# Kernel tuning notes

Measured on AMD Instinct MI355X. Metric: run time of the kernel, lower is better.

## Reference

```python
import jax, jax.numpy as jnp
import numpy as np

B, H, T, DH = 2, 16, 2048, 64
SCALE = DH ** -0.5


def setup_inputs() -> dict:
    key = jax.random.key(0)
    kq, kk, kv = jax.random.split(key, 3)
    q = jax.random.normal(kq, (B, H, T, DH), dtype=jnp.float32)
    k = jax.random.normal(kk, (B, H, T, DH), dtype=jnp.float32)
    v = jax.random.normal(kv, (B, H, T, DH), dtype=jnp.float32)
    attention_mask = jnp.ones((B, T), dtype=bool)  # (B, Tk) padding mask, True=keep
    causal_mask = jnp.tril(jnp.ones((T, T), dtype=bool))[None, None]  # (1,1,Tq,Tk)
    return {"q": q, "k": k, "v": v, "attention_mask": attention_mask,
            "causal_mask": causal_mask}


def _attend(q, k, v, attention_mask, causal_mask):
    # scores in fp32 as in the torch module
    scores = jnp.einsum("bhqd,bhkd->bhqk", q.astype(jnp.float32),
                        k.astype(jnp.float32)) * SCALE
    neg_inf = jnp.float32(-jnp.inf)
    # (B,Tk) bool padding mask -> (B,1,1,Tk), broadcasts over Tq
    pad = attention_mask[:, None, None, :]
    scores = jnp.where(pad, scores, neg_inf)
    scores = jnp.where(causal_mask, scores, neg_inf)
    attn = jax.nn.softmax(scores, axis=-1).astype(q.dtype)
    ctx = jnp.einsum("bhqk,bhkd->bhqd", attn, v)  # (B,H,Tq,Dh)
    Bq, Hq, Tq, Dh = ctx.shape
    return ctx.transpose(0, 2, 1, 3).reshape(Bq, Tq, Hq * Dh)


def reference(q, k, v, attention_mask, causal_mask):
    return _attend(q, k, v, attention_mask, causal_mask)
```

## Files before the change

kernel.cpp:

```cpp
#include <hip/hip_runtime.h>


constexpr int Bc = 2, Hc = 16, Tc = 2048, Dc = 64;
constexpr float QSCALE = 0.125f * 1.44269504088896340736f;

typedef __attribute__((__ext_vector_type__(8))) __bf16 bf16x8;
typedef __attribute__((__ext_vector_type__(4))) __bf16 bf16x4;
typedef __attribute__((__ext_vector_type__(4))) float f32x4;

__global__ __launch_bounds__(256, 4) void attn_fwd_kernel(
    const float* __restrict__ Q,
    const float* __restrict__ K,
    const float* __restrict__ V,
    float* __restrict__ O)
{
  const int tid  = threadIdx.x;
  const int wave = tid >> 6;
  const int lane = tid & 63;
  const int l16  = lane & 15;
  const int g    = lane >> 4;

  const int bid  = blockIdx.x;
  const int head = bid & 31;
  const int pr   = bid >> 5;
  const int b = head >> 4, h = head & 15;

  const size_t hoff = (size_t)head * Tc * Dc;
  const float* Qb = Q + hoff;
  const float* Kb = K + hoff;
  const float* Vb = V + hoff;

  __shared__ __bf16 Kl[64 * 64];
  __shared__ __bf16 Vt[64 * 64];

  const int krow = tid >> 2;
  const int seg  = tid & 3;
  const int kswz = (krow & 7) << 4;
  const int vkb  = tid >> 4;
  const int vdb  = tid & 15;
  const int vwx  = (vdb >> 2) << 3;

  float4 kreg[4], vreg[4];

  for (int ph = 0; ph < 2; ++ph) {
    const int qtile = ph ? (31 - pr) : pr;
    const int q0 = qtile * 64 + wave * 16;

    bf16x8 qf[2];
    {
      const float4* qp = (const float4*)(Qb + (size_t)(q0 + l16) * Dc + g * 8);
      #pragma unroll
      for (int c = 0; c < 2; ++c) {
        float4 x0 = qp[c * 8], x1 = qp[c * 8 + 1];
        const float* f0 = (const float*)&x0;
        const float* f1 = (const float*)&x1;
        #pragma unroll
        for (int j = 0; j < 4; ++j) {
          qf[c][j]     = (__bf16)(f0[j] * QSCALE);
          qf[c][4 + j] = (__bf16)(f1[j] * QSCALE);
        }
      }
    }

    f32x4 o_acc[4] = {};
    float m_run = -1e30f, l_run = 0.f;

    const int n_iter = qtile + 1;

    {
      const float4* kp4 = (const float4*)(Kb + (size_t)krow * Dc + seg * 16);
      #pragma unroll
      for (int c = 0; c < 4; ++c) kreg[c] = kp4[c];
      const float* vb0 = Vb + (size_t)(vkb * 4) * Dc + vdb * 4;
      #pragma unroll
      for (int r = 0; r < 4; ++r) vreg[r] = *(const float4*)(vb0 + r * Dc);
    }

    for (int it = 0; it < n_iter; ++it) {
      __syncthreads();

      #pragma unroll
      for (int hh = 0; hh < 2; ++hh) {
        const float* x0 = (const float*)&kreg[2 * hh];
        const float* x1 = (const float*)&kreg[2 * hh + 1];
        bf16x8 t;
        #pragma unroll
        for (int j = 0; j < 4; ++j) { t[j] = (__bf16)x0[j]; t[4 + j] = (__bf16)x1[j]; }
        *(bf16x8*)((char*)Kl + krow * 128 + ((seg * 32 + hh * 16) ^ kswz)) = t;
      }
      #pragma unroll
      for (int i = 0; i < 4; ++i) {
        bf16x4 t;
        #pragma unroll
        for (int r = 0; r < 4; ++r) t[r] = (__bf16)((const float*)&vreg[r])[i];
        const int d = vdb * 4 + i;
        *(bf16x4*)((char*)Vt + vkb * 512 + ((d * 8) ^ (vkb << 3) ^ vwx)) = t;
      }
      __syncthreads();

      if (it + 1 < n_iter) {
        const int kv1 = (it + 1) * 64;
        const float4* kp4 = (const float4*)(Kb + (size_t)(kv1 + krow) * Dc + seg * 16);
        #pragma unroll
        for (int c = 0; c < 4; ++c) kreg[c] = kp4[c];
        const float* vb0 = Vb + (size_t)(kv1 + vkb * 4) * Dc + vdb * 4;
        #pragma unroll
        for (int r = 0; r < 4; ++r) vreg[r] = *(const float4*)(vb0 + r * Dc);
      }

      const bool partial = (it == qtile);
      const int  ns = partial ? (wave + 1) : 4;

      f32x4 sacc[4];
      __builtin_amdgcn_s_setprio(1);
      #pragma unroll
      for (int s = 0; s < 4; ++s) {
        if (s < ns) {
          f32x4 z = {0.f, 0.f, 0.f, 0.f};
          const int row = s * 16 + l16;
          const char* kb = (const char*)Kl + row * 128;
          const int swz = (row & 7) << 4;
          bf16x8 k0 = *(const bf16x8*)(kb + ((g * 16) ^ swz));
          bf16x8 k1 = *(const bf16x8*)(kb + ((64 + g * 16) ^ swz));
          z = __builtin_amdgcn_mfma_f32_16x16x32_bf16(k0, qf[0], z, 0, 0, 0);
          z = __builtin_amdgcn_mfma_f32_16x16x32_bf16(k1, qf[1], z, 0, 0, 0);
          sacc[s] = z;
        } else {
          sacc[s] = f32x4{-INFINITY, -INFINITY, -INFINITY, -INFINITY};
        }
      }
      __builtin_amdgcn_s_setprio(0);
      if (partial) {
        #pragma unroll
        for (int s = 0; s < 4; ++s)
          #pragma unroll
          for (int r = 0; r < 4; ++r)
            if (s * 16 + g * 4 + r > wave * 16 + l16) sacc[s][r] = -INFINITY;
      }

      float mx = -INFINITY;
      #pragma unroll
      for (int s = 0; s < 4; ++s)
        #pragma unroll
        for (int r = 0; r < 4; ++r) mx = fmaxf(mx, sacc[s][r]);
      mx = fmaxf(mx, __shfl_xor(mx, 16, 64));
      mx = fmaxf(mx, __shfl_xor(mx, 32, 64));

      if (!__all(mx <= m_run + 8.0f)) {
        const float mn = fmaxf(m_run, mx);
        const float f  = __builtin_amdgcn_exp2f(m_run - mn);
        m_run = mn;
        l_run *= f;
        #pragma unroll
        for (int r = 0; r < 4; ++r) {
          const float fo = __shfl(f, g * 4 + r, 64);
          #pragma unroll
          for (int dt = 0; dt < 4; ++dt) o_acc[dt][r] *= fo;
        }
      }

      float sum = 0.f;
      bf16x8 pa[2];
      #pragma unroll
      for (int c = 0; c < 2; ++c)
        #pragma unroll
        for (int j = 0; j < 8; ++j) {
          const float pv = __builtin_amdgcn_exp2f(sacc[2 * c + (j >> 2)][j & 3] - m_run);
          sum += pv;
          pa[c][j] = (__bf16)pv;
        }
      sum += __shfl_xor(sum, 16, 64);
      sum += __shfl_xor(sum, 32, 64);
      l_run += sum;

      __builtin_amdgcn_s_setprio(1);
      #pragma unroll
      for (int dt = 0; dt < 4; ++dt) {
        const int d = dt * 16 + l16;
        const int dx = (dt & 3) << 3;
        #pragma unroll
        for (int c = 0; c < 2; ++c) {
          const int kc0 = 8 * c + g;
          const int kc1 = 8 * c + 4 + g;
          union { bf16x8 v8; bf16x4 v4[2]; } u;
          u.v4[0] = *(const bf16x4*)((char*)Vt + kc0 * 512 + ((d * 8) ^ (kc0 << 3) ^ dx));
          u.v4[1] = *(const bf16x4*)((char*)Vt + kc1 * 512 + ((d * 8) ^ (kc1 << 3) ^ dx));
          o_acc[dt] = __builtin_amdgcn_mfma_f32_16x16x32_bf16(pa[c], u.v8, o_acc[dt], 0, 0, 0);
        }
      }
      __builtin_amdgcn_s_setprio(0);
    }

    #pragma unroll
    for (int r = 0; r < 4; ++r) {
      const float il = __shfl(l_run, g * 4 + r, 64);
      const float inv = 1.f / il;
      float* orow = O + ((size_t)b * Tc + (q0 + g * 4 + r)) * (Hc * Dc) + h * Dc;
      #pragma unroll
      for (int dt = 0; dt < 4; ++dt)
        orow[dt * 16 + l16] = o_acc[dt][r] * inv;
    }
  }
}

extern "C" void kernel_launch(void* const* d_in, const int* in_sizes, int n_in,
                              void* d_out, int out_size, void* d_ws, size_t ws_size,
                              hipStream_t stream) {
  const float* q = (const float*)d_in[0];
  const float* k = (const float*)d_in[1];
  const float* v = (const float*)d_in[2];
  float* out = (float*)d_out;

  dim3 grid(512);
  dim3 block(256);
  hipLaunchKernelGGL(attn_fwd_kernel, grid, block, 0, stream, q, k, v, out);
}
```

Before: 53.09 us.

## Double-buffer K/V in LDS and launch one q-tile per block

Replaces the paired-tile scheme (each block processed tile pr and 31-pr) with one q-tile per block, giving 1024 blocks with the heaviest tiles scheduled first. Adds ping-pong LDS buffers for K and V so the bf16 conversion and store of the next tile happens after compute on the current one, cutting one __syncthreads per iteration. This doubles LDS use per block, which may limit occupancy, and relies on the hardware scheduler rather than explicit pairing for causal load balance.

```diff
diff --git a/kernel.cpp b/kernel.cpp
--- a/kernel.cpp
+++ b/kernel.cpp
@@ -20,18 +20,19 @@
   const int l16  = lane & 15;
   const int g    = lane >> 4;
 
-  const int bid  = blockIdx.x;
-  const int head = bid & 31;
-  const int pr   = bid >> 5;
+  const int bid   = blockIdx.x;
+  const int head  = bid & 31;
+  const int qtile = 31 - (bid >> 5);
   const int b = head >> 4, h = head & 15;
+  const int q0 = qtile * 64 + wave * 16;
 
   const size_t hoff = (size_t)head * Tc * Dc;
   const float* Qb = Q + hoff;
   const float* Kb = K + hoff;
   const float* Vb = V + hoff;
 
-  __shared__ __bf16 Kl[64 * 64];
-  __shared__ __bf16 Vt[64 * 64];
+  __shared__ __bf16 Kl[2][64 * 64];
+  __shared__ __bf16 Vt[2][64 * 64];
 
   const int krow = tid >> 2;
   const int seg  = tid & 3;
@@ -40,45 +41,154 @@
   const int vdb  = tid & 15;
   const int vwx  = (vdb >> 2) << 3;
 
+  bf16x8 qf[2];
+  {
+    const float4* qp = (const float4*)(Qb + (size_t)(q0 + l16) * Dc + g * 8);
+    #pragma unroll
+    for (int c = 0; c < 2; ++c) {
+      float4 x0 = qp[c * 8], x1 = qp[c * 8 + 1];
+      const float* f0 = (const float*)&x0;
+      const float* f1 = (const float*)&x1;
+      #pragma unroll
+      for (int j = 0; j < 4; ++j) {
+        qf[c][j]     = (__bf16)(f0[j] * QSCALE);
+        qf[c][4 + j] = (__bf16)(f1[j] * QSCALE);
+      }
+    }
+  }
+
+  f32x4 o_acc[4] = {};
+  float m_run = -1e30f, l_run = 0.f;
+
+  const int n_iter = qtile + 1;
   float4 kreg[4], vreg[4];
 
-  for (int ph = 0; ph < 2; ++ph) {
-    const int qtile = ph ? (31 - pr) : pr;
-    const int q0 = qtile * 64 + wave * 16;
-
-    bf16x8 qf[2];
-    {
-      const float4* qp = (const float4*)(Qb + (size_t)(q0 + l16) * Dc + g * 8);
+  {
+    const float4* kp4 = (const float4*)(Kb + (size_t)krow * Dc + seg * 16);
+    #pragma unroll
+    for (int c = 0; c < 4; ++c) kreg[c] = kp4[c];
+    const float* vb0 = Vb + (size_t)(vkb * 4) * Dc + vdb * 4;
+    #pragma unroll
+    for (int r = 0; r < 4; ++r) vreg[r] = *(const float4*)(vb0 + r * Dc);
+
+    #pragma unroll
+    for (int hh = 0; hh < 2; ++hh) {
+      const float* x0 = (const float*)&kreg[2 * hh];
+      const float* x1 = (const float*)&kreg[2 * hh + 1];
+      bf16x8 t;
+      #pragma unroll
+      for (int j = 0; j < 4; ++j) { t[j] = (__bf16)x0[j]; t[4 + j] = (__bf16)x1[j]; }
+      *(bf16x8*)((char*)Kl[0] + krow * 128 + ((seg * 32 + hh * 16) ^ kswz)) = t;
+    }
+    #pragma unroll
+    for (int i = 0; i < 4; ++i) {
+      bf16x4 t;
+      #pragma unroll
+      for (int r = 0; r < 4; ++r) t[r] = (__bf16)((const float*)&vreg[r])[i];
+      const int d = vdb * 4 + i;
+      *(bf16x4*)((char*)Vt[0] + vkb * 512 + ((d * 8) ^ (vkb << 3) ^ vwx)) = t;
+    }
+  }
+
+  for (int it = 0; it < n_iter; ++it) {
+    __syncthreads();
+    const int cur = it & 1;
+
+    const bool more = (it + 1 < n_iter);
+    if (more) {
+      const int kv1 = (it + 1) * 64;
+      const float4* kp4 = (const float4*)(Kb + (size_t)(kv1 + krow) * Dc + seg * 16);
+      #pragma unroll
+      for (int c = 0; c < 4; ++c) kreg[c] = kp4[c];
+      const float* vb0 = Vb + (size_t)(kv1 + vkb * 4) * Dc + vdb * 4;
+      #pragma unroll
+      for (int r = 0; r < 4; ++r) vreg[r] = *(const float4*)(vb0 + r * Dc);
+    }
+
+    const bool partial = (it == qtile);
+    const int  ns = partial ? (wave + 1) : 4;
+
+    f32x4 sacc[4];
+    __builtin_amdgcn_s_setprio(1);
+    #pragma unroll
+    for (int s = 0; s < 4; ++s) {
+      if (s < ns) {
+        f32x4 z = {0.f, 0.f, 0.f, 0.f};
+        const int row = s * 16 + l16;
+        const char* kb = (const char*)Kl[cur] + row * 128;
+        const int swz = (row & 7) << 4;
+        bf16x8 k0 = *(const bf16x8*)(kb + ((g * 16) ^ swz));
+        bf16x8 k1 = *(const bf16x8*)(kb + ((64 + g * 16) ^ swz));
+        z = __builtin_amdgcn_mfma_f32_16x16x32_bf16(k0, qf[0], z, 0, 0, 0);
+        z = __builtin_amdgcn_mfma_f32_16x16x32_bf16(k1, qf[1], z, 0, 0, 0);
+        sacc[s] = z;
+      } else {
+        sacc[s] = f32x4{-INFINITY, -INFINITY, -INFINITY, -INFINITY};
+      }
+    }
+    __builtin_amdgcn_s_setprio(0);
+    if (partial) {
+      #pragma unroll
+      for (int s = 0; s < 4; ++s)
+        #pragma unroll
+        for (int r = 0; r < 4; ++r)
+          if (s * 16 + g * 4 + r > wave * 16 + l16) sacc[s][r] = -INFINITY;
+    }
+
+    float mx = -INFINITY;
+    #pragma unroll
+    for (int s = 0; s < 4; ++s)
+      #pragma unroll
+      for (int r = 0; r < 4; ++r) mx = fmaxf(mx, sacc[s][r]);
+    mx = fmaxf(mx, __shfl_xor(mx, 16, 64));
+    mx = fmaxf(mx, __shfl_xor(mx, 32, 64));
+
+    if (!__all(mx <= m_run + 8.0f)) {
+      const float mn = fmaxf(m_run, mx);
+      const float f  = __builtin_amdgcn_exp2f(m_run - mn);
+      m_run = mn;
+      l_run *= f;
+      #pragma unroll
+      for (int r = 0; r < 4; ++r) {
+        const float fo = __shfl(f, g * 4 + r, 64);
+        #pragma unroll
+        for (int dt = 0; dt < 4; ++dt) o_acc[dt][r] *= fo;
+      }
+    }
+
+    float sum = 0.f;
+    bf16x8 pa[2];
+    #pragma unroll
+    for (int c = 0; c < 2; ++c)
+      #pragma unroll
+      for (int j = 0; j < 8; ++j) {
+        const float pv = __builtin_amdgcn_exp2f(sacc[2 * c + (j >> 2)][j & 3] - m_run);
+        sum += pv;
+        pa[c][j] = (__bf16)pv;
+      }
+    sum += __shfl_xor(sum, 16, 64);
+    sum += __shfl_xor(sum, 32, 64);
+    l_run += sum;
+
+    __builtin_amdgcn_s_setprio(1);
+    #pragma unroll
+    for (int dt = 0; dt < 4; ++dt) {
+      const int d = dt * 16 + l16;
+      const int dx = (dt & 3) << 3;
       #pragma unroll
       for (int c = 0; c < 2; ++c) {
-        float4 x0 = qp[c * 8], x1 = qp[c * 8 + 1];
-        const float* f0 = (const float*)&x0;
-        const float* f1 = (const float*)&x1;
-        #pragma unroll
-        for (int j = 0; j < 4; ++j) {
-          qf[c][j]     = (__bf16)(f0[j] * QSCALE);
-          qf[c][4 + j] = (__bf16)(f1[j] * QSCALE);
-        }
-      }
-    }
-
-    f32x4 o_acc[4] = {};
-    float m_run = -1e30f, l_run = 0.f;
-
-    const int n_iter = qtile + 1;
-
-    {
-      const float4* kp4 = (const float4*)(Kb + (size_t)krow * Dc + seg * 16);
-      #pragma unroll
-      for (int c = 0; c < 4; ++c) kreg[c] = kp4[c];
-      const float* vb0 = Vb + (size_t)(vkb * 4) * Dc + vdb * 4;
-      #pragma unroll
-      for (int r = 0; r < 4; ++r) vreg[r] = *(const float4*)(vb0 + r * Dc);
-    }
-
-    for (int it = 0; it < n_iter; ++it) {
-      __syncthreads();
-
+        const int kc0 = 8 * c + g;
+        const int kc1 = 8 * c + 4 + g;
+        union { bf16x8 v8; bf16x4 v4[2]; } u;
+        u.v4[0] = *(const bf16x4*)((char*)Vt[cur] + kc0 * 512 + ((d * 8) ^ (kc0 << 3) ^ dx));
+        u.v4[1] = *(const bf16x4*)((char*)Vt[cur] + kc1 * 512 + ((d * 8) ^ (kc1 << 3) ^ dx));
+        o_acc[dt] = __builtin_amdgcn_mfma_f32_16x16x32_bf16(pa[c], u.v8, o_acc[dt], 0, 0, 0);
+      }
+    }
+    __builtin_amdgcn_s_setprio(0);
+
+    if (more) {
+      const int nxt = cur ^ 1;
       #pragma unroll
       for (int hh = 0; hh < 2; ++hh) {
         const float* x0 = (const float*)&kreg[2 * hh];
@@ -86,7 +196,7 @@
         bf16x8 t;
         #pragma unroll
         for (int j = 0; j < 4; ++j) { t[j] = (__bf16)x0[j]; t[4 + j] = (__bf16)x1[j]; }
-        *(bf16x8*)((char*)Kl + krow * 128 + ((seg * 32 + hh * 16) ^ kswz)) = t;
+        *(bf16x8*)((char*)Kl[nxt] + krow * 128 + ((seg * 32 + hh * 16) ^ kswz)) = t;
       }
       #pragma unroll
       for (int i = 0; i < 4; ++i) {
@@ -94,112 +204,19 @@
         #pragma unroll
         for (int r = 0; r < 4; ++r) t[r] = (__bf16)((const float*)&vreg[r])[i];
         const int d = vdb * 4 + i;
-        *(bf16x4*)((char*)Vt + vkb * 512 + ((d * 8) ^ (vkb << 3) ^ vwx)) = t;
-      }
-      __syncthreads();
-
-      if (it + 1 < n_iter) {
-        const int kv1 = (it + 1) * 64;
-        const float4* kp4 = (const float4*)(Kb + (size_t)(kv1 + krow) * Dc + seg * 16);
-        #pragma unroll
-        for (int c = 0; c < 4; ++c) kreg[c] = kp4[c];
-        const float* vb0 = Vb + (size_t)(kv1 + vkb * 4) * Dc + vdb * 4;
-        #pragma unroll
-        for (int r = 0; r < 4; ++r) vreg[r] = *(const float4*)(vb0 + r * Dc);
-      }
-
-      const bool partial = (it == qtile);
-      const int  ns = partial ? (wave + 1) : 4;
-
-      f32x4 sacc[4];
-      __builtin_amdgcn_s_setprio(1);
-      #pragma unroll
-      for (int s = 0; s < 4; ++s) {
-        if (s < ns) {
-          f32x4 z = {0.f, 0.f, 0.f, 0.f};
-          const int row = s * 16 + l16;
-          const char* kb = (const char*)Kl + row * 128;
-          const int swz = (row & 7) << 4;
-          bf16x8 k0 = *(const bf16x8*)(kb + ((g * 16) ^ swz));
-          bf16x8 k1 = *(const bf16x8*)(kb + ((64 + g * 16) ^ swz));
-          z = __builtin_amdgcn_mfma_f32_16x16x32_bf16(k0, qf[0], z, 0, 0, 0);
-          z = __builtin_amdgcn_mfma_f32_16x16x32_bf16(k1, qf[1], z, 0, 0, 0);
-          sacc[s] = z;
-        } else {
-          sacc[s] = f32x4{-INFINITY, -INFINITY, -INFINITY, -INFINITY};
-        }
-      }
-      __builtin_amdgcn_s_setprio(0);
-      if (partial) {
-        #pragma unroll
-        for (int s = 0; s < 4; ++s)
-          #pragma unroll
-          for (int r = 0; r < 4; ++r)
-            if (s * 16 + g * 4 + r > wave * 16 + l16) sacc[s][r] = -INFINITY;
-      }
-
-      float mx = -INFINITY;
-      #pragma unroll
-      for (int s = 0; s < 4; ++s)
-        #pragma unroll
-        for (int r = 0; r < 4; ++r) mx = fmaxf(mx, sacc[s][r]);
-      mx = fmaxf(mx, __shfl_xor(mx, 16, 64));
-      mx = fmaxf(mx, __shfl_xor(mx, 32, 64));
-
-      if (!__all(mx <= m_run + 8.0f)) {
-        const float mn = fmaxf(m_run, mx);
-        const float f  = __builtin_amdgcn_exp2f(m_run - mn);
-        m_run = mn;
-        l_run *= f;
-        #pragma unroll
-        for (int r = 0; r < 4; ++r) {
-          const float fo = __shfl(f, g * 4 + r, 64);
-          #pragma unroll
-          for (int dt = 0; dt < 4; ++dt) o_acc[dt][r] *= fo;
-        }
-      }
-
-      float sum = 0.f;
-      bf16x8 pa[2];
-      #pragma unroll
-      for (int c = 0; c < 2; ++c)
-        #pragma unroll
-        for (int j = 0; j < 8; ++j) {
-          const float pv = __builtin_amdgcn_exp2f(sacc[2 * c + (j >> 2)][j & 3] - m_run);
-          sum += pv;
-          pa[c][j] = (__bf16)pv;
-        }
-      sum += __shfl_xor(sum, 16, 64);
-      sum += __shfl_xor(sum, 32, 64);
-      l_run += sum;
-
-      __builtin_amdgcn_s_setprio(1);
-      #pragma unroll
-      for (int dt = 0; dt < 4; ++dt) {
-        const int d = dt * 16 + l16;
-        const int dx = (dt & 3) << 3;
-        #pragma unroll
-        for (int c = 0; c < 2; ++c) {
-          const int kc0 = 8 * c + g;
-          const int kc1 = 8 * c + 4 + g;
-          union { bf16x8 v8; bf16x4 v4[2]; } u;
-          u.v4[0] = *(const bf16x4*)((char*)Vt + kc0 * 512 + ((d * 8) ^ (kc0 << 3) ^ dx));
-          u.v4[1] = *(const bf16x4*)((char*)Vt + kc1 * 512 + ((d * 8) ^ (kc1 << 3) ^ dx));
-          o_acc[dt] = __builtin_amdgcn_mfma_f32_16x16x32_bf16(pa[c], u.v8, o_acc[dt], 0, 0, 0);
-        }
-      }
-      __builtin_amdgcn_s_setprio(0);
-    }
-
-    #pragma unroll
-    for (int r = 0; r < 4; ++r) {
-      const float il = __shfl(l_run, g * 4 + r, 64);
-      const float inv = 1.f / il;
-      float* orow = O + ((size_t)b * Tc + (q0 + g * 4 + r)) * (Hc * Dc) + h * Dc;
-      #pragma unroll
-      for (int dt = 0; dt < 4; ++dt)
-        orow[dt * 16 + l16] = o_acc[dt][r] * inv;
-    }
+        *(bf16x4*)((char*)Vt[nxt] + vkb * 512 + ((d * 8) ^ (vkb << 3) ^ vwx)) = t;
+      }
+    }
+  }
+
+  #pragma unroll
+  for (int r = 0; r < 4; ++r) {
+    const float il = __shfl(l_run, g * 4 + r, 64);
+    const float inv = 1.f / il;
+    float* orow = O + ((size_t)b * Tc + (q0 + g * 4 + r)) * (Hc * Dc) + h * Dc;
+    #pragma unroll
+    for (int dt = 0; dt < 4; ++dt)
+      orow[dt * 16 + l16] = o_acc[dt][r] * inv;
   }
 }
 
@@ -211,7 +228,7 @@
   const float* v = (const float*)d_in[2];
   float* out = (float*)d_out;
 
-  dim3 grid(512);
+  dim3 grid(1024);
   dim3 block(256);
   hipLaunchKernelGGL(attn_fwd_kernel, grid, block, 0, stream, q, k, v, out);
 }
```

After: 49.31 us. 7.1% less time.
